# Optimization experiments

Measured on AMD Instinct MI355X. Metric: run time of the kernel, lower is better.

## Reference

```python
import jax, jax.numpy as jnp
import numpy as np

B, N, E = 32, 2048, 1048576  # 32 uniform graphs of 2048 nodes, avg degree 16
BN = B * N
KS = (1024, 512, 256)  # TopKPooling ratio=0.5 -> ceil(0.5*n) per layer (uniform graphs -> static)


def _mlp2(x, w1, b1, w2, b2):
    # nn.Sequential(Linear, ReLU, Linear)
    return jnp.maximum(x @ w1 + b1, 0.0) @ w2 + b2


def _forward(x, edge_attr, node_w1, node_b1, node_w2, node_b2,
             edge_w1, edge_b1, edge_w2, edge_b2,
             eff_in_w, eff_in_b, eff_h_w, eff_h_b, eff_out_w, eff_out_b,
             upd_in_w, upd_in_b, upd_h_w, upd_h_b, upd_out_w, upd_out_b,
             pool_w, edge_index):
    relu = lambda t: jnp.maximum(t, 0.0)
    src, dst = edge_index[0], edge_index[1]  # PyG: x_j = h[src], x_i = h[dst], aggregate at dst
    h = _mlp2(x, node_w1, node_b1, node_w2, node_b2)          # [BN, F] node embedding
    e = _mlp2(edge_attr, edge_w1, edge_b1, edge_w2, edge_b2)  # [E, F]  edge embedding
    node_mask = jnp.ones((BN,), bool)
    edge_mask = jnp.ones((E,), bool)
    for i in range(3):
        # --- DPIGNNLayer: gather-concat-MLP(+edge_attr) message, scatter-mean aggregate ---
        m = jnp.concatenate([h[dst], h[src]], axis=-1)        # [E, 2F] = cat(x_i, x_j)
        m = relu(m @ eff_in_w[i] + eff_in_b[i])
        m = relu(m @ eff_h_w[i] + eff_h_b[i])
        m = relu(m @ eff_out_w[i] + eff_out_b[i] + e)
        em = edge_mask.astype(h.dtype)[:, None]
        agg = jax.ops.segment_sum(m * em, dst, num_segments=BN)
        cnt = jax.ops.segment_sum(em, dst, num_segments=BN)
        mean = agg / jnp.maximum(cnt, 1.0)                    # mean aggr (0 where no edges)
        u = jnp.concatenate([mean, h], axis=-1)
        u = relu(u @ upd_in_w[i] + upd_in_b[i])
        u = relu(u @ upd_h_w[i] + upd_h_b[i])
        _ = relu(u @ upd_out_w[i] + upd_out_b[i] + h)  # dead compute: source update() returns x
        # --- TopKPooling(ratio=0.5), masked form (uniform graph sizes -> static k) ---
        w = pool_w[i]
        score = jnp.tanh((h @ w) / jnp.linalg.norm(w))        # [BN]
        masked = jnp.where(node_mask, score, -jnp.inf).reshape(B, N)
        _, idx = jax.lax.top_k(masked, KS[i])                 # [B, k]
        sel = jnp.zeros((B, N), bool).at[jnp.arange(B)[:, None], idx].set(True).reshape(-1)
        node_mask = sel
        h = jnp.where(node_mask[:, None], h * score[:, None], 0.0)
        edge_mask = edge_mask & node_mask[src] & node_mask[dst]  # filter_adj equivalent
    # global_mean_pool over surviving nodes per graph
    nm = node_mask.astype(h.dtype)[:, None]
    sums = (h * nm).reshape(B, N, -1).sum(axis=1)
    cnts = nm.reshape(B, N, 1).sum(axis=1)
    return sums / jnp.maximum(cnts, 1.0)  # [B, F]


def setup_inputs() -> dict:
    key = jax.random.key(0)
    ks = iter(jax.random.split(key, 40))
    F, ND, ED = 128, 16, 8
    s = 0.05
    W = lambda shape: jax.random.normal(next(ks), shape, jnp.float32) * s
    zb = lambda shape: jnp.zeros(shape, jnp.float32)
    e_per = E // B
    base = (jnp.arange(E) // e_per) * N  # graph offset per edge
    src = jax.random.randint(next(ks), (E,), 0, N) + base
    dst = jax.random.randint(next(ks), (E,), 0, N) + base
    return {
        'x': jax.random.normal(next(ks), (BN, ND), jnp.float32),
        'edge_attr': jax.random.normal(next(ks), (E, ED), jnp.float32),
        'node_w1': W((ND, F)), 'node_b1': zb((F,)),
        'node_w2': W((F, F)), 'node_b2': zb((F,)),
        'edge_w1': W((ED, F)), 'edge_b1': zb((F,)),
        'edge_w2': W((F, F)), 'edge_b2': zb((F,)),
        'eff_in_w': W((3, 2 * F, F)), 'eff_in_b': zb((3, F)),
        'eff_h_w': W((3, F, F)), 'eff_h_b': zb((3, F)),
        'eff_out_w': W((3, F, F)), 'eff_out_b': zb((3, F)),
        'upd_in_w': W((3, 2 * F, F)), 'upd_in_b': zb((3, F)),
        'upd_h_w': W((3, F, F)), 'upd_h_b': zb((3, F)),
        'upd_out_w': W((3, F, F)), 'upd_out_b': zb((3, F)),
        'pool_w': W((3, F)),
        'edge_index': jnp.stack([src, dst]),
    }


def reference(x, edge_attr, node_w1, node_b1, node_w2, node_b2,
              edge_w1, edge_b1, edge_w2, edge_b2,
              eff_in_w, eff_in_b, eff_h_w, eff_h_b, eff_out_w, eff_out_b,
              upd_in_w, upd_in_b, upd_h_w, upd_h_b, upd_out_w, upd_out_b,
              pool_w, edge_index):
    return _forward(x, edge_attr, node_w1, node_b1, node_w2, node_b2,
                    edge_w1, edge_b1, edge_w2, edge_b2,
                    eff_in_w, eff_in_b, eff_h_w, eff_h_b, eff_out_w, eff_out_b,
                    upd_in_w, upd_in_b, upd_h_w, upd_h_b, upd_out_w, upd_out_b,
                    pool_w, edge_index)
```

## Files before the change

kernel.cpp:

```cpp
#include <hip/hip_runtime.h>
#include <hip/hip_bf16.h>


#define NPG    2048
#define NGRAPH 32
#define HP     2112
#define HPAD(b) ((b) + ((b) >> 5))

__global__ __launch_bounds__(256) void k1_fused(
    const float* __restrict__ x,
    const float* __restrict__ W1,
    const float* __restrict__ b1,
    const float* __restrict__ W2,
    const float* __restrict__ b2,
    const float* __restrict__ pw,
    float4* __restrict__ d4)
{
    __shared__ float4 sW1v[512];
    __shared__ float4 sb1v[32];
    __shared__ __align__(16) float swn[384];
    __shared__ __align__(16) float sv[384];
    __shared__ float sc[4];
    __shared__ float snorm[3];
    int t = threadIdx.x;
    int lane = t & 63, wv = t >> 6;

    for (int i = t; i < 512; i += 256) sW1v[i] = ((const float4*)W1)[i];
    if (t < 32) sb1v[t] = ((const float4*)b1)[t];
    if (wv < 3) {
        float w0 = pw[wv * 128 + lane];
        float w1 = pw[wv * 128 + 64 + lane];
        float p = w0 * w0 + w1 * w1;
        #pragma unroll
        for (int s = 32; s; s >>= 1) p += __shfl_xor(p, s);
        if (lane == 0) snorm[wv] = sqrtf(p);
    }
    __syncthreads();
    for (int i = t; i < 384; i += 256) swn[i] = pw[i] / snorm[i >> 7];
    __syncthreads();
    for (int task = t; task < 387; task += 256) {
        int k = task / 129, j = task % 129;
        const float4* r4 = (const float4*)((j < 128) ? (W2 + j * 128) : b2);
        const float* wn = swn + k * 128;
        float p0 = 0.f, p1 = 0.f, p2 = 0.f, p3 = 0.f;
        #pragma unroll 8
        for (int q = 0; q < 32; ++q) {
            float4 w = r4[q];
            p0 = fmaf(w.x, wn[4 * q + 0], p0);
            p1 = fmaf(w.y, wn[4 * q + 1], p1);
            p2 = fmaf(w.z, wn[4 * q + 2], p2);
            p3 = fmaf(w.w, wn[4 * q + 3], p3);
        }
        float p = (p0 + p1) + (p2 + p3);
        if (j < 128) sv[k * 128 + j] = p;
        else sc[k] = p;
    }
    __syncthreads();

    int n = blockIdx.x * 256 + t;
    const float4* xr = (const float4*)(x + (size_t)n * 16);
    float4 xa = xr[0], xb = xr[1], xc = xr[2], xd = xr[3];
    float xs[16] = {xa.x, xa.y, xa.z, xa.w, xb.x, xb.y, xb.z, xb.w,
                    xc.x, xc.y, xc.z, xc.w, xd.x, xd.y, xd.z, xd.w};
    const float4* sv4 = (const float4*)sv;
    float dd0 = sc[0], dd1 = sc[1], dd2 = sc[2];
    #pragma unroll 4
    for (int fq = 0; fq < 32; ++fq) {
        float4 a4 = sb1v[fq];
        #pragma unroll
        for (int j = 0; j < 16; ++j) {
            float4 w = sW1v[j * 32 + fq];
            a4.x = fmaf(xs[j], w.x, a4.x);
            a4.y = fmaf(xs[j], w.y, a4.y);
            a4.z = fmaf(xs[j], w.z, a4.z);
            a4.w = fmaf(xs[j], w.w, a4.w);
        }
        a4.x = fmaxf(a4.x, 0.f); a4.y = fmaxf(a4.y, 0.f);
        a4.z = fmaxf(a4.z, 0.f); a4.w = fmaxf(a4.w, 0.f);
        float4 v0 = sv4[fq], v1 = sv4[32 + fq], v2 = sv4[64 + fq];
        dd0 = fmaf(a4.x, v0.x, fmaf(a4.y, v0.y, fmaf(a4.z, v0.z, fmaf(a4.w, v0.w, dd0))));
        dd1 = fmaf(a4.x, v1.x, fmaf(a4.y, v1.y, fmaf(a4.z, v1.z, fmaf(a4.w, v1.w, dd1))));
        dd2 = fmaf(a4.x, v2.x, fmaf(a4.y, v2.y, fmaf(a4.z, v2.z, fmaf(a4.w, v2.w, dd2))));
    }
    d4[n] = make_float4(dd0, dd1, dd2, 0.f);
}

__global__ __launch_bounds__(1024, 1) void k2_cascade(
    const float* __restrict__ x,
    const float* __restrict__ W1,
    const float* __restrict__ b1,
    const float* __restrict__ W2,
    const float* __restrict__ b2,
    const float4* __restrict__ d4,
    float* __restrict__ out)
{
    __shared__ float d0A[NPG], d1A[NPG], d2A[NPG];
    __shared__ unsigned long long sKey[NPG];
    __shared__ unsigned int hist[2][HP];
    __shared__ int   idxB[1024];
    __shared__ float cscB[1024], d1B[1024], d2B[1024];
    __shared__ int   idxA2[512];
    __shared__ float cscA2[512], d2A2[512];
    __shared__ float sW1[2048], sb1[128];
    __shared__ float Spart[1024], Svec[128], red4[4];
    __shared__ unsigned long long sPrefix;
    __shared__ int sNeed, sDone, sCnt;

    int t = threadIdx.x, g = blockIdx.x;
    int lane = t & 63, wv = t >> 6;

    for (int n = t; n < NPG; n += 1024) {
        float4 dd = d4[g * NPG + n];
        d0A[n] = dd.x; d1A[n] = dd.y; d2A[n] = dd.z;
    }
    for (int i = t; i < 2048; i += 1024) sW1[i] = W1[i];
    if (t < 128) sb1[t] = b1[t];
    for (int i = t; i < 2 * HP; i += 1024) ((unsigned int*)hist)[i] = 0u;
    __syncthreads();

    int curN = NPG;
    for (int r = 0; r < 3; ++r) {
        int kk = 1024 >> r;
        const float* dIn   = (r == 0) ? d0A : (r == 1) ? d1B : d2A2;
        const float* cscIn = (r == 0) ? (const float*)0 : (r == 1) ? cscB : cscA2;
        const int*   idxIn = (r == 0) ? (const int*)0 : (r == 1) ? idxB : idxA2;
        int*   idxOut = (r == 1) ? idxA2 : idxB;
        float* cscOut = (r == 1) ? cscA2 : cscB;

        if (t == 0) { sPrefix = 0ull; sNeed = kk; sDone = 0; sCnt = 0; }
        for (int m = t; m < curN; m += 1024) {
            float ci = cscIn ? cscIn[m] : 1.f;
            int   ni = idxIn ? idxIn[m] : m;
            float z = ci * dIn[m];
            unsigned int bb = __float_as_uint(z);
            unsigned int mo = (bb & 0x80000000u) ? ~bb : (bb | 0x80000000u);
            unsigned long long kv = ((unsigned long long)mo << 11)
                                  | (unsigned long long)(unsigned int)(2047 - ni);
            sKey[m] = kv;
            atomicAdd(&hist[0][HPAD((unsigned int)(kv >> 33) & 2047u)], 1u);
        }
        __syncthreads();

        int lastBuf = 0;
        for (int pass = 0; pass < 4; ++pass) {
            int buf = pass & 1;
            int shift = 33 - 11 * pass;
            lastBuf = buf;
            if (pass > 0) {
                unsigned long long pref = sPrefix;
                for (int m = t; m < curN; m += 1024) {
                    unsigned long long kv = sKey[m];
                    if ((kv >> (shift + 11)) == (pref >> (shift + 11)))
                        atomicAdd(&hist[buf][HPAD((unsigned int)(kv >> shift) & 2047u)], 1u);
                }
                __syncthreads();
            }
            if (wv == 0) {
                unsigned long long pref = sPrefix;
                unsigned int need = (unsigned int)sNeed;
                unsigned int h[32], tl = 0;
                #pragma unroll
                for (int b = 0; b < 32; ++b) {
                    h[b] = hist[buf][HPAD(32u * t + b)];
                    tl += h[b];
                }
                unsigned int s = tl;
                #pragma unroll
                for (int d = 1; d < 64; d <<= 1) {
                    unsigned int v = __shfl_down(s, d);
                    if (t + d < 64) s += v;
                }
                unsigned int above = s - tl;
                if (above < need && above + tl >= need) {
                    unsigned int cum = above;
                    #pragma unroll
                    for (int b = 31; b >= 0; --b) {
                        cum += h[b];
                        if (cum >= need) {
                            int nn = (int)(need - (cum - h[b]));
                            sNeed = nn;
                            sPrefix = pref |
                                ((unsigned long long)(unsigned int)(32 * t + b) << shift);
                            sDone = (nn == (int)h[b]) || (pass == 3);
                            break;
                        }
                    }
                }
            } else if (pass > 0) {
                for (int i = t - 64; i < HP; i += 960) hist[buf ^ 1][i] = 0u;
            }
            __syncthreads();
            if (sDone) break;
        }
        unsigned long long thr = sPrefix;

        for (int i = t; i < HP; i += 1024) hist[lastBuf][i] = 0u;
        for (int m = t; m < curN; m += 1024) {
            unsigned long long kv = sKey[m];
            bool pred = (kv >= thr);
            unsigned long long mask = __ballot(pred);
            if (mask) {
                int leader = __ffsll((long long)mask) - 1;
                int cnt = __popcll(mask);
                int base = 0;
                if (lane == leader) base = atomicAdd(&sCnt, cnt);
                base = __shfl(base, leader);
                if (pred) {
                    int rank = __popcll(mask & ((1ull << lane) - 1ull));
                    int pos = base + rank;
                    float ci = cscIn ? cscIn[m] : 1.f;
                    int   ni = idxIn ? idxIn[m] : m;
                    float z = ci * dIn[m];
                    idxOut[pos] = ni;
                    cscOut[pos] = ci * tanhf(z);
                    if (r == 0)      { d1B[pos] = d1A[m]; d2B[pos] = d2A[m]; }
                    else if (r == 1) { d2A2[pos] = d2B[m]; }
                }
            }
        }
        __syncthreads();
        curN = kk;
    }

    {
        int f = t & 127, grp = t >> 7;
        float Sacc = 0.f;
        for (int it = grp; it < 256; it += 8) {
            int n = idxB[it];
            float cn = cscB[it];
            const float4* xr = (const float4*)(x + (size_t)(g * NPG + n) * 16);
            float4 xa = xr[0], xb = xr[1], xc = xr[2], xd = xr[3];
            float acc = sb1[f];
            acc = fmaf(xa.x, sW1[0 * 128 + f], acc);
            acc = fmaf(xa.y, sW1[1 * 128 + f], acc);
            acc = fmaf(xa.z, sW1[2 * 128 + f], acc);
            acc = fmaf(xa.w, sW1[3 * 128 + f], acc);
            acc = fmaf(xb.x, sW1[4 * 128 + f], acc);
            acc = fmaf(xb.y, sW1[5 * 128 + f], acc);
            acc = fmaf(xb.z, sW1[6 * 128 + f], acc);
            acc = fmaf(xb.w, sW1[7 * 128 + f], acc);
            acc = fmaf(xc.x, sW1[8 * 128 + f], acc);
            acc = fmaf(xc.y, sW1[9 * 128 + f], acc);
            acc = fmaf(xc.z, sW1[10 * 128 + f], acc);
            acc = fmaf(xc.w, sW1[11 * 128 + f], acc);
            acc = fmaf(xd.x, sW1[12 * 128 + f], acc);
            acc = fmaf(xd.y, sW1[13 * 128 + f], acc);
            acc = fmaf(xd.z, sW1[14 * 128 + f], acc);
            acc = fmaf(xd.w, sW1[15 * 128 + f], acc);
            Sacc += fmaxf(acc, 0.f) * cn;
        }
        Spart[t] = Sacc;
    }
    if (t < 256) {
        float cpart = cscB[t];
        #pragma unroll
        for (int s = 32; s; s >>= 1) cpart += __shfl_xor(cpart, s);
        if ((t & 63) == 0) red4[t >> 6] = cpart;
    }
    __syncthreads();
    if (t < 128) {
        float sv = 0.f;
        #pragma unroll
        for (int h = 0; h < 8; ++h) sv += Spart[h * 128 + t];
        Svec[t] = sv;
    }
    __syncthreads();
    if (t < 128) {
        float Csum = (red4[0] + red4[1]) + (red4[2] + red4[3]);
        float acc = Csum * b2[t];
        for (int j = 0; j < 128; ++j)
            acc = fmaf(Svec[j], W2[j * 128 + t], acc);
        out[g * 128 + t] = acc * (1.0f / 256.0f);
    }
}

extern "C" void kernel_launch(void* const* d_in, const int* in_sizes, int n_in,
                              void* d_out, int out_size, void* d_ws, size_t ws_size,
                              hipStream_t stream) {
    const float* x  = (const float*)d_in[0];
    const float* W1 = (const float*)d_in[2];
    const float* b1 = (const float*)d_in[3];
    const float* W2 = (const float*)d_in[4];
    const float* b2 = (const float*)d_in[5];
    const float* pw = (const float*)d_in[22];
    float* out = (float*)d_out;

    float4* d4 = (float4*)d_ws;

    k1_fused<<<256, 256, 0, stream>>>(x, W1, b1, W2, b2, pw, d4);
    k2_cascade<<<NGRAPH, 1024, 0, stream>>>(x, W1, b1, W2, b2, d4, out);
}
```

Baseline: 168.2 us.

## Build first-round top-k radix histogram in node kernel via global atomics

The first radix-select histogram pass for layer 0 moves into k1, which does a global atomicAdd per node into a per-graph 2048-bin histogram cleared by a memset. k2 no longer stages all 2048 d-values in shared memory; it re-reads d4 from global for refinement passes and the compaction. The final W2 matvec is split across 8 thread groups with a shared-memory reduction, and the gather loop is unrolled by 2. This costs an extra memset launch and global atomic contention in exchange for a shorter serial prologue in the 32-block cascade kernel.

```diff
diff --git a/kernel.cpp b/kernel.cpp
--- a/kernel.cpp
+++ b/kernel.cpp
@@ -6,6 +6,11 @@
 #define NGRAPH 32
 #define HP     2112
 #define HPAD(b) ((b) + ((b) >> 5))
+
+__device__ __forceinline__ unsigned int mono_bits(float z) {
+    unsigned int bb = __float_as_uint(z);
+    return (bb & 0x80000000u) ? ~bb : (bb | 0x80000000u);
+}
 
 __global__ __launch_bounds__(256) void k1_fused(
     const float* __restrict__ x,
@@ -14,7 +19,8 @@
     const float* __restrict__ W2,
     const float* __restrict__ b2,
     const float* __restrict__ pw,
-    float4* __restrict__ d4)
+    float4* __restrict__ d4,
+    unsigned int* __restrict__ ghist)
 {
     __shared__ float4 sW1v[512];
     __shared__ float4 sb1v[32];
@@ -83,6 +89,7 @@
         dd2 = fmaf(a4.x, v2.x, fmaf(a4.y, v2.y, fmaf(a4.z, v2.z, fmaf(a4.w, v2.w, dd2))));
     }
     d4[n] = make_float4(dd0, dd1, dd2, 0.f);
+    atomicAdd(&ghist[(n >> 11) * 2048 + (mono_bits(dd0) >> 22)], 1u);
 }
 
 __global__ __launch_bounds__(1024, 1) void k2_cascade(
@@ -92,10 +99,10 @@
     const float* __restrict__ W2,
     const float* __restrict__ b2,
     const float4* __restrict__ d4,
+    const unsigned int* __restrict__ ghist,
     float* __restrict__ out)
 {
-    __shared__ float d0A[NPG], d1A[NPG], d2A[NPG];
-    __shared__ unsigned long long sKey[NPG];
+    __shared__ unsigned long long sKey[1024];
     __shared__ unsigned int hist[2][HP];
     __shared__ int   idxB[1024];
     __shared__ float cscB[1024], d1B[1024], d2B[1024];
@@ -108,40 +115,147 @@
 
     int t = threadIdx.x, g = blockIdx.x;
     int lane = t & 63, wv = t >> 6;
-
-    for (int n = t; n < NPG; n += 1024) {
-        float4 dd = d4[g * NPG + n];
-        d0A[n] = dd.x; d1A[n] = dd.y; d2A[n] = dd.z;
-    }
+    const float4* d4g = d4 + (size_t)g * NPG;
+
     for (int i = t; i < 2048; i += 1024) sW1[i] = W1[i];
     if (t < 128) sb1[t] = b1[t];
     for (int i = t; i < 2 * HP; i += 1024) ((unsigned int*)hist)[i] = 0u;
-    __syncthreads();
-
-    int curN = NPG;
-    for (int r = 0; r < 3; ++r) {
+    if (t == 0) { sPrefix = 0ull; sNeed = 1024; sDone = 0; sCnt = 0; }
+    __syncthreads();
+
+    if (wv == 0) {
+        const uint4* gh = (const uint4*)(ghist + (size_t)g * 2048 + 32 * t);
+        unsigned int h[32], tl = 0;
+        #pragma unroll
+        for (int i = 0; i < 8; ++i) {
+            uint4 q = gh[i];
+            h[4 * i + 0] = q.x; h[4 * i + 1] = q.y;
+            h[4 * i + 2] = q.z; h[4 * i + 3] = q.w;
+            tl += q.x + q.y + q.z + q.w;
+        }
+        unsigned int need = 1024u;
+        unsigned int s = tl;
+        #pragma unroll
+        for (int d = 1; d < 64; d <<= 1) {
+            unsigned int v = __shfl_down(s, d);
+            if (t + d < 64) s += v;
+        }
+        unsigned int above = s - tl;
+        if (above < need && above + tl >= need) {
+            unsigned int cum = above;
+            #pragma unroll
+            for (int b = 31; b >= 0; --b) {
+                cum += h[b];
+                if (cum >= need) {
+                    int nn = (int)(need - (cum - h[b]));
+                    sNeed = nn;
+                    sPrefix = (unsigned long long)(unsigned int)(32 * t + b) << 33;
+                    sDone = (nn == (int)h[b]);
+                    break;
+                }
+            }
+        }
+    }
+    __syncthreads();
+    int lastBuf = -1;
+    for (int pass = 1; pass < 4 && !sDone; ++pass) {
+        int buf = pass & 1;
+        int shift = 33 - 11 * pass;
+        lastBuf = buf;
+        unsigned long long pref = sPrefix;
+        for (int m = t; m < NPG; m += 1024) {
+            unsigned long long kv =
+                ((unsigned long long)mono_bits(d4g[m].x) << 11)
+                | (unsigned long long)(unsigned int)(2047 - m);
+            if ((kv >> (shift + 11)) == (pref >> (shift + 11)))
+                atomicAdd(&hist[buf][HPAD((unsigned int)(kv >> shift) & 2047u)], 1u);
+        }
+        __syncthreads();
+        if (wv == 0) {
+            unsigned int need = (unsigned int)sNeed;
+            unsigned int h[32], tl = 0;
+            #pragma unroll
+            for (int b = 0; b < 32; ++b) {
+                h[b] = hist[buf][HPAD(32u * t + b)];
+                tl += h[b];
+            }
+            unsigned int s = tl;
+            #pragma unroll
+            for (int d = 1; d < 64; d <<= 1) {
+                unsigned int v = __shfl_down(s, d);
+                if (t + d < 64) s += v;
+            }
+            unsigned int above = s - tl;
+            if (above < need && above + tl >= need) {
+                unsigned int cum = above;
+                #pragma unroll
+                for (int b = 31; b >= 0; --b) {
+                    cum += h[b];
+                    if (cum >= need) {
+                        int nn = (int)(need - (cum - h[b]));
+                        sNeed = nn;
+                        sPrefix = pref |
+                            ((unsigned long long)(unsigned int)(32 * t + b) << shift);
+                        sDone = (nn == (int)h[b]) || (pass == 3);
+                        break;
+                    }
+                }
+            }
+        } else if (pass >= 2) {
+            for (int i = t - 64; i < HP; i += 960) hist[buf ^ 1][i] = 0u;
+        }
+        __syncthreads();
+    }
+    {
+        unsigned long long thr = sPrefix;
+        if (lastBuf >= 0)
+            for (int i = t; i < HP; i += 1024) hist[lastBuf][i] = 0u;
+        for (int m = t; m < NPG; m += 1024) {
+            float4 dd = d4g[m];
+            unsigned long long kv =
+                ((unsigned long long)mono_bits(dd.x) << 11)
+                | (unsigned long long)(unsigned int)(2047 - m);
+            bool pred = (kv >= thr);
+            unsigned long long mask = __ballot(pred);
+            if (mask) {
+                int leader = __ffsll((long long)mask) - 1;
+                int cnt = __popcll(mask);
+                int base = 0;
+                if (lane == leader) base = atomicAdd(&sCnt, cnt);
+                base = __shfl(base, leader);
+                if (pred) {
+                    int rank = __popcll(mask & ((1ull << lane) - 1ull));
+                    int pos = base + rank;
+                    idxB[pos] = m;
+                    cscB[pos] = tanhf(dd.x);
+                    d1B[pos] = dd.y;
+                    d2B[pos] = dd.z;
+                }
+            }
+        }
+        __syncthreads();
+    }
+
+    int curN = 1024;
+    for (int r = 1; r < 3; ++r) {
         int kk = 1024 >> r;
-        const float* dIn   = (r == 0) ? d0A : (r == 1) ? d1B : d2A2;
-        const float* cscIn = (r == 0) ? (const float*)0 : (r == 1) ? cscB : cscA2;
-        const int*   idxIn = (r == 0) ? (const int*)0 : (r == 1) ? idxB : idxA2;
+        const float* dIn   = (r == 1) ? d1B : d2A2;
+        const float* cscIn = (r == 1) ? cscB : cscA2;
+        const int*   idxIn = (r == 1) ? idxB : idxA2;
         int*   idxOut = (r == 1) ? idxA2 : idxB;
         float* cscOut = (r == 1) ? cscA2 : cscB;
 
         if (t == 0) { sPrefix = 0ull; sNeed = kk; sDone = 0; sCnt = 0; }
         for (int m = t; m < curN; m += 1024) {
-            float ci = cscIn ? cscIn[m] : 1.f;
-            int   ni = idxIn ? idxIn[m] : m;
-            float z = ci * dIn[m];
-            unsigned int bb = __float_as_uint(z);
-            unsigned int mo = (bb & 0x80000000u) ? ~bb : (bb | 0x80000000u);
-            unsigned long long kv = ((unsigned long long)mo << 11)
-                                  | (unsigned long long)(unsigned int)(2047 - ni);
+            float z = cscIn[m] * dIn[m];
+            unsigned long long kv = ((unsigned long long)mono_bits(z) << 11)
+                | (unsigned long long)(unsigned int)(2047 - idxIn[m]);
             sKey[m] = kv;
             atomicAdd(&hist[0][HPAD((unsigned int)(kv >> 33) & 2047u)], 1u);
         }
         __syncthreads();
 
-        int lastBuf = 0;
+        lastBuf = 0;
         for (int pass = 0; pass < 4; ++pass) {
             int buf = pass & 1;
             int shift = 33 - 11 * pass;
@@ -208,13 +322,10 @@
                 if (pred) {
                     int rank = __popcll(mask & ((1ull << lane) - 1ull));
                     int pos = base + rank;
-                    float ci = cscIn ? cscIn[m] : 1.f;
-                    int   ni = idxIn ? idxIn[m] : m;
-                    float z = ci * dIn[m];
-                    idxOut[pos] = ni;
-                    cscOut[pos] = ci * tanhf(z);
-                    if (r == 0)      { d1B[pos] = d1A[m]; d2B[pos] = d2A[m]; }
-                    else if (r == 1) { d2A2[pos] = d2B[m]; }
+                    float ci = cscIn[m];
+                    idxOut[pos] = idxIn[m];
+                    cscOut[pos] = ci * tanhf(ci * dIn[m]);
+                    if (r == 1) d2A2[pos] = d2B[m];
                 }
             }
         }
@@ -225,6 +336,7 @@
     {
         int f = t & 127, grp = t >> 7;
         float Sacc = 0.f;
+        #pragma unroll 2
         for (int it = grp; it < 256; it += 8) {
             int n = idxB[it];
             float cn = cscB[it];
@@ -265,11 +377,20 @@
         Svec[t] = sv;
     }
     __syncthreads();
+    {
+        int f = t & 127, jc = t >> 7;
+        float part = 0.f;
+        #pragma unroll
+        for (int j = 16 * jc; j < 16 * jc + 16; ++j)
+            part = fmaf(Svec[j], W2[j * 128 + f], part);
+        Spart[t] = part;
+    }
+    __syncthreads();
     if (t < 128) {
         float Csum = (red4[0] + red4[1]) + (red4[2] + red4[3]);
         float acc = Csum * b2[t];
-        for (int j = 0; j < 128; ++j)
-            acc = fmaf(Svec[j], W2[j * 128 + t], acc);
+        #pragma unroll
+        for (int h = 0; h < 8; ++h) acc += Spart[h * 128 + t];
         out[g * 128 + t] = acc * (1.0f / 256.0f);
     }
 }
@@ -286,7 +407,9 @@
     float* out = (float*)d_out;
 
     float4* d4 = (float4*)d_ws;
-
-    k1_fused<<<256, 256, 0, stream>>>(x, W1, b1, W2, b2, pw, d4);
-    k2_cascade<<<NGRAPH, 1024, 0, stream>>>(x, W1, b1, W2, b2, d4, out);
+    unsigned int* ghist = (unsigned int*)((char*)d_ws + (1 << 20));
+
+    hipMemsetAsync(ghist, 0, NGRAPH * 2048 * sizeof(unsigned int), stream);
+    k1_fused<<<256, 256, 0, stream>>>(x, W1, b1, W2, b2, pw, d4, ghist);
+    k2_cascade<<<NGRAPH, 1024, 0, stream>>>(x, W1, b1, W2, b2, d4, ghist, out);
 }
```

Measured after the change: 175.7 us. 4.5% more time.
